# Kernel optimization log

Measured on AMD Instinct MI355X. Metric: run time of the kernel, lower is better.

## Reference

```python
import jax
import jax.numpy as jnp
import numpy as np
from jax import lax

B, NS, T, H, V = 4, 96, 8, 256, 32000
L = NS * T
N = NS + 1                    # num_nodes = num_statements + 1 (exit node)
NUM_LAYERS = NS // 16         # avg_statements_per_step = 16 -> 6 execution steps


def _lstm(c, h, x, Wx, Wh, b):
    """flax-style LSTM cell: gates in (i, f, g, o) order."""
    z = x @ Wx + h @ Wh + b
    gi, gf, gg, go = jnp.split(z, 4, axis=-1)
    c2 = jax.nn.sigmoid(gf) * c + jax.nn.sigmoid(gi) * jnp.tanh(gg)
    h2 = jax.nn.sigmoid(go) * jnp.tanh(c2)
    return c2, h2


def _forward(code_statements, code_length, embed, Wx_s, Wh_s, b_s, W_se, b_se,
             Wx_e, Wh_e, b_e, W_hk, b_hk, W_sd, b_sd, W_d1, b_d1, init_a, init_b):
    # ---- statement embedding: LSTM over the T tokens of each statement ----
    tok = embed[code_statements.astype(jnp.int32)]            # [B, L, H]
    tok = jnp.transpose(tok.reshape(B * NS, T, H), (1, 0, 2))  # [T, B*NS, H]
    c0 = jnp.zeros((B * NS, H), tok.dtype)

    def scan_fn(carry, x):
        c, hh = carry
        c, hh = _lstm(c, hh, x, Wx_s, Wh_s, b_s)
        return (c, hh), None

    (_, h_last), _ = lax.scan(scan_fn, (c0, c0), tok)
    stmt = h_last.reshape(B, NS, H)                           # [B, NS, H]

    # ---- skip encoder: pairwise segment-sum embedding for skipping i -> j ----
    node = jnp.concatenate([stmt, jnp.zeros((B, 1, H), stmt.dtype)], axis=1)  # [B,N,H]
    pref = jnp.concatenate(
        [jnp.zeros((B, 1, H), stmt.dtype), jnp.cumsum(node, axis=1)], axis=1)[:, :N]
    skip = (pref[:, None, :, :] - pref[:, :, None, :]) @ W_se + b_se  # [B,N,N,H]

    stmt_len = (code_length // T).astype(jnp.int32)           # exit node index per example

    # ---- execution loop with soft instruction pointer ----
    c = jnp.broadcast_to(init_a, (B, N, H))
    h = jnp.broadcast_to(init_b, (B, N, H))
    p = jnp.zeros((B, N)).at[:, 0].set(1.0)

    def step(c, h, p, skip_nnh, length, layer):
        # per-example: c,h [N,H]; p [N]; skip_nnh [N,N,H]; length scalar
        n = p.shape[0]
        ar = jnp.arange(n)
        if layer == 0:
            mask = jnp.zeros((n, n)).at[:, 1].set(1.0)
        elif layer == NUM_LAYERS - 1:
            mask = jnp.zeros((n, n)).at[:, length].set(1.0)   # force skip to exit
        else:
            mask = 1.0 - jnp.tri(n)                           # strictly forward skips
            mask = jnp.where(ar <= length, mask, 0.0)         # no skips past exit
            mask = mask.at[:, length].set(1.0)                # always allow exit

        # skip attention logits
        skip_keys = skip_nnh @ W_sd + b_sd                    # [N,N,H]
        h_key = h @ W_hk + b_hk                               # [N,H]
        act = jax.nn.relu(jnp.concatenate(
            [jnp.broadcast_to(h_key[:, None, :], (n, n, H)), skip_keys], axis=-1))
        skip_logits = jnp.squeeze(act @ W_d1, -1) + b_d1[0]   # [N,N]
        skip_logits = jnp.where(mask > 0, skip_logits, -jnp.inf)
        skip_p = jax.nn.softmax(skip_logits, axis=-1)

        # one LSTM skip-execution step for every (i, j) pair, vectorized
        z = skip_nnh @ Wx_e + (h @ Wh_e)[:, None, :] + b_e    # [N,N,4H]
        gi, gf, gg, go = jnp.split(z, 4, axis=-1)
        c_prop = jax.nn.sigmoid(gf) * c[:, None, :] + jax.nn.sigmoid(gi) * jnp.tanh(gg)
        h_prop = jax.nn.sigmoid(go) * jnp.tanh(c_prop)
        fwd_edge = (ar[None, :] > ar[:, None])[:, :, None]    # only j > i executes
        c_prop = jnp.where(fwd_edge, c_prop, c[:, None, :])
        h_prop = jnp.where(fwd_edge, h_prop, h[:, None, :])
        valid = (mask[:, :, None] > 0) & (p[:, None, None] > 0)
        c_prop = jnp.where(valid, c_prop, 0.0)
        h_prop = jnp.where(valid, h_prop, 0.0)

        # soft aggregation of proposals weighted by p(i) * skip_p(i -> j)
        w = skip_p * p[:, None]                               # [N,N]
        denom = (w.sum(axis=0) + 1e-7)[:, None]               # [N,1]
        c_new = jnp.einsum('ijh,ij->jh', c_prop, w) / denom
        h_new = jnp.einsum('ijh,ij->jh', h_prop, w) / denom
        p_new = p @ skip_p
        return c_new, h_new, p_new

    for layer in range(NUM_LAYERS):
        c, h, p = jax.vmap(step, in_axes=(0, 0, 0, 0, 0, None))(
            c, h, p, skip, stmt_len, layer)
    return h                                                  # [B, N, H]


def setup_inputs() -> dict:
    key = jax.random.key(0)
    ks = jax.random.split(key, 16)

    def dense(k, fi, fo):
        return jax.random.normal(k, (fi, fo)) * (1.0 / np.sqrt(fi))

    return {
        'code_statements': jax.random.randint(ks[0], (B, L), 0, V, dtype=jnp.int32),
        'code_length': jax.random.randint(ks[1], (B,), 64, L, dtype=jnp.int32),
        'embed': jax.random.normal(ks[2], (V, H)) * 0.02,
        'Wx_s': dense(ks[3], H, 4 * H), 'Wh_s': dense(ks[4], H, 4 * H),
        'b_s': jnp.zeros((4 * H,)),
        'W_se': dense(ks[5], H, H), 'b_se': jnp.zeros((H,)),
        'Wx_e': dense(ks[6], H, 4 * H), 'Wh_e': dense(ks[7], H, 4 * H),
        'b_e': jnp.zeros((4 * H,)),
        'W_hk': dense(ks[8], H, H), 'b_hk': jnp.zeros((H,)),
        'W_sd': dense(ks[9], H, H), 'b_sd': jnp.zeros((H,)),
        'W_d1': dense(ks[10], 2 * H, 1), 'b_d1': jnp.zeros((1,)),
        'init_a': jax.random.normal(ks[11], (H,)),
        'init_b': jax.random.normal(ks[12], (H,)),
    }


def reference(code_statements, code_length, embed, Wx_s, Wh_s, b_s, W_se, b_se,
              Wx_e, Wh_e, b_e, W_hk, b_hk, W_sd, b_sd, W_d1, b_d1, init_a, init_b):
    return _forward(code_statements, code_length, embed, Wx_s, Wh_s, b_s, W_se, b_se,
                    Wx_e, Wh_e, b_e, W_hk, b_hk, W_sd, b_sd, W_d1, b_d1, init_a, init_b)
```

## Files before the change

### kernel.cpp

```cpp
#include <hip/hip_runtime.h>
#include <cstddef>

#define B_   4
#define NS_  96
#define T_   8
#define H_   256
#define N_   97
#define NL_  6
#define R_   388

__device__ __forceinline__ float sigm(float x) {
    return __builtin_amdgcn_rcpf(1.0f + __builtin_amdgcn_exp2f(-1.44269504f * x));
}
__device__ __forceinline__ float tanh_f(float x) {
    return 1.0f - 2.0f * __builtin_amdgcn_rcpf(1.0f + __builtin_amdgcn_exp2f(2.88539008f * x));
}

__device__ __forceinline__ void fma16(float4 a, float4 w0, float4 w1, float4 w2,
                                      float4 w3, float* acc) {
    acc[0] = fmaf(a.x, w0.x, acc[0]); acc[1] = fmaf(a.x, w0.y, acc[1]);
    acc[2] = fmaf(a.x, w0.z, acc[2]); acc[3] = fmaf(a.x, w0.w, acc[3]);
    acc[0] = fmaf(a.y, w1.x, acc[0]); acc[1] = fmaf(a.y, w1.y, acc[1]);
    acc[2] = fmaf(a.y, w1.z, acc[2]); acc[3] = fmaf(a.y, w1.w, acc[3]);
    acc[0] = fmaf(a.z, w2.x, acc[0]); acc[1] = fmaf(a.z, w2.y, acc[1]);
    acc[2] = fmaf(a.z, w2.z, acc[2]); acc[3] = fmaf(a.z, w2.w, acc[3]);
    acc[0] = fmaf(a.w, w3.x, acc[0]); acc[1] = fmaf(a.w, w3.y, acc[1]);
    acc[2] = fmaf(a.w, w3.z, acc[2]); acc[3] = fmaf(a.w, w3.w, acc[3]);
}

__global__ __launch_bounds__(512, 4) void prologue(
        const int* __restrict__ ids, const float* __restrict__ embed,
        const float* __restrict__ Wx_s, const float* __restrict__ b_s,
        const float* __restrict__ b_se, const float* __restrict__ Wx_e,
        const float* __restrict__ b_e, const float* __restrict__ W_sd,
        const float* __restrict__ b_sd, const float* __restrict__ Wh_e,
        const float* __restrict__ init_a, const float* __restrict__ init_b,
        float* __restrict__ xz, float* __restrict__ cz, float* __restrict__ ck,
        float* __restrict__ hw, float* __restrict__ c0, float* __restrict__ h0,
        float* __restrict__ p0) {
    int bid = blockIdx.x, t = threadIdx.x;
    if (bid < 384) {
        __shared__ float As[64][260];
        __shared__ int ridx[64];
        int r0 = (bid >> 3) * 64, n0 = (bid & 7) * 128;
        if (t < 64) ridx[t] = ids[r0 + t];
        __syncthreads();
#pragma unroll
        for (int m = 0; m < 8; m++) {
            int L = m * 512 + t;
            int r = L >> 6, c4 = (L & 63) * 4;
            *(float4*)&As[r][c4] = *(const float4*)(embed + (size_t)ridx[r] * 256 + c4);
        }
        __syncthreads();
        int rg = t >> 5, cg = t & 31;
        float acc[4][4] = {};
        const float* wp = Wx_s + n0 + 4 * cg;
#pragma unroll 4
        for (int kb = 0; kb < 64; kb++) {
            float4 w0 = *(const float4*)(wp + (size_t)(4 * kb + 0) * 1024);
            float4 w1 = *(const float4*)(wp + (size_t)(4 * kb + 1) * 1024);
            float4 w2 = *(const float4*)(wp + (size_t)(4 * kb + 2) * 1024);
            float4 w3 = *(const float4*)(wp + (size_t)(4 * kb + 3) * 1024);
#pragma unroll
            for (int i = 0; i < 4; i++) {
                float4 a = *(const float4*)&As[rg * 4 + i][4 * kb];
                fma16(a, w0, w1, w2, w3, acc[i]);
            }
        }
        int col = n0 + 4 * cg;
        float4 bv = *(const float4*)&b_s[col];
#pragma unroll
        for (int i = 0; i < 4; i++) {
            int r = r0 + rg * 4 + i;
            float4 o = make_float4(acc[i][0] + bv.x, acc[i][1] + bv.y,
                                   acc[i][2] + bv.z, acc[i][3] + bv.w);
            *(float4*)&xz[(size_t)r * 1024 + col] = o;
        }
    } else if (bid < 386) {
        int n = (bid - 384) * 512 + t;
        float acc = b_e[n];
        for (int k = 0; k < 256; k++) acc = fmaf(b_se[k], Wx_e[(size_t)k * 1024 + n], acc);
        cz[n] = acc;
    } else if (bid < 388) {
        int n = (bid - 386) * 512 + t;
        float acc = b_e[n];
        for (int k = 0; k < 256; k++) {
            acc = fmaf(b_se[k], Wx_e[(size_t)k * 1024 + n], acc);
            acc = fmaf(init_b[k], Wh_e[(size_t)k * 1024 + n], acc);
        }
        hw[n] = acc;
    } else if (bid == 388) {
        if (t < 256) {
            float acc = b_sd[t];
            for (int k = 0; k < 256; k++) acc = fmaf(b_se[k], W_sd[(size_t)k * 256 + t], acc);
            ck[t] = acc;
        }
    } else {
        int r0 = (bid - 389) * 8 + (t >> 8) * 4;
        int col = t & 255;
        float ia = init_a[col], ib = init_b[col];
#pragma unroll
        for (int rr = 0; rr < 4; rr++) {
            int row = r0 + rr;
            if (row < R_) {
                c0[(size_t)row * 256 + col] = ia;
                h0[(size_t)row * 256 + col] = ib;
                if (col == 0) p0[row] = ((row % N_) == 0) ? 1.0f : 0.0f;
            }
        }
    }
}

__global__ __launch_bounds__(1024) void lstm_onepass(const float* __restrict__ xz,
        const float* __restrict__ Wh, float* __restrict__ hbuf) {
    __shared__ float zpart[4][2][1024];
    __shared__ float h_s[2][260];
    __shared__ float Wh_c[28][1024];
    int t = threadIdx.x;
    int s0 = blockIdx.x * 2;
    int kg = t >> 8, tg = t & 255;
    int sg = (t >> 8) & 1, cc = t & 255;
#pragma unroll
    for (int m = 0; m < 7; m++) {
        int L = m * 1024 + t;
        int r = L >> 8, c4 = (L & 255) * 4;
        *(float4*)&Wh_c[r][c4] = *(const float4*)(Wh + (size_t)r * 1024 + c4);
    }
    float creg = 0.0f, hreg = 0.0f;
    if (t < 512) {
        const float* z0 = xz + ((size_t)(s0 + sg) * T_) * 1024;
        float gi = z0[cc], gg = z0[512 + cc], go = z0[768 + cc];
        creg = sigm(gi) * tanh_f(gg);
        hreg = sigm(go) * tanh_f(creg);
        h_s[sg][cc] = hreg;
    }
    __syncthreads();
    for (int step = 1; step < T_; step++) {
        float x0 = 0.f, x1 = 0.f, x2 = 0.f, x3 = 0.f;
        if (t < 512) {
            const float* xzp = xz + ((size_t)(s0 + sg) * T_ + step) * 1024;
            x0 = xzp[cc]; x1 = xzp[256 + cc]; x2 = xzp[512 + cc]; x3 = xzp[768 + cc];
        }
        float4 z[2] = {};
        const float* wp = Wh + (size_t)(kg * 64) * 1024 + 4 * tg;
        int kbase = kg * 64;
        if (kg == 0) {
#pragma unroll
            for (int kb = 0; kb < 7; kb++) {
                float4 w0 = *(const float4*)&Wh_c[4 * kb + 0][4 * tg];
                float4 w1 = *(const float4*)&Wh_c[4 * kb + 1][4 * tg];
                float4 w2 = *(const float4*)&Wh_c[4 * kb + 2][4 * tg];
                float4 w3 = *(const float4*)&Wh_c[4 * kb + 3][4 * tg];
                int k = 4 * kb;
#pragma unroll
                for (int s = 0; s < 2; s++) {
                    float4 a = *(const float4*)&h_s[s][k];
                    fma16(a, w0, w1, w2, w3, (float*)&z[s]);
                }
            }
#pragma unroll 3
            for (int kb = 7; kb < 16; kb++) {
                float4 w0 = *(const float4*)(wp + (size_t)(4 * kb + 0) * 1024);
                float4 w1 = *(const float4*)(wp + (size_t)(4 * kb + 1) * 1024);
                float4 w2 = *(const float4*)(wp + (size_t)(4 * kb + 2) * 1024);
                float4 w3 = *(const float4*)(wp + (size_t)(4 * kb + 3) * 1024);
                int k = 4 * kb;
#pragma unroll
                for (int s = 0; s < 2; s++) {
                    float4 a = *(const float4*)&h_s[s][k];
                    fma16(a, w0, w1, w2, w3, (float*)&z[s]);
                }
            }
        } else {
#pragma unroll 4
            for (int kb = 0; kb < 16; kb++) {
                float4 w0 = *(const float4*)(wp + (size_t)(4 * kb + 0) * 1024);
                float4 w1 = *(const float4*)(wp + (size_t)(4 * kb + 1) * 1024);
                float4 w2 = *(const float4*)(wp + (size_t)(4 * kb + 2) * 1024);
                float4 w3 = *(const float4*)(wp + (size_t)(4 * kb + 3) * 1024);
                int k = kbase + 4 * kb;
#pragma unroll
                for (int s = 0; s < 2; s++) {
                    float4 a = *(const float4*)&h_s[s][k];
                    fma16(a, w0, w1, w2, w3, (float*)&z[s]);
                }
            }
        }
#pragma unroll
        for (int s = 0; s < 2; s++)
            *(float4*)&zpart[kg][s][4 * tg] = z[s];
        __syncthreads();
        if (t < 512) {
            float zv0 = x0 + zpart[0][sg][cc] + zpart[1][sg][cc]
                      + zpart[2][sg][cc] + zpart[3][sg][cc];
            float zv1 = x1 + zpart[0][sg][256 + cc] + zpart[1][sg][256 + cc]
                      + zpart[2][sg][256 + cc] + zpart[3][sg][256 + cc];
            float zv2 = x2 + zpart[0][sg][512 + cc] + zpart[1][sg][512 + cc]
                      + zpart[2][sg][512 + cc] + zpart[3][sg][512 + cc];
            float zv3 = x3 + zpart[0][sg][768 + cc] + zpart[1][sg][768 + cc]
                      + zpart[2][sg][768 + cc] + zpart[3][sg][768 + cc];
            creg = sigm(zv1) * creg + sigm(zv0) * tanh_f(zv2);
            hreg = sigm(zv3) * tanh_f(creg);
            h_s[sg][cc] = hreg;
        }
        __syncthreads();
    }
    if (t < 512) hbuf[(size_t)(s0 + sg) * H_ + cc] = hreg;
}

template<int MT>
__global__ __launch_bounds__(256) void gemm_t(const float* __restrict__ A,
        const float* __restrict__ W, const float* __restrict__ bias,
        const float* __restrict__ subQ, const float* __restrict__ pgate,
        float* __restrict__ C, int R, int NC) {
    __shared__ float As[MT][260];
    __shared__ int anyflag;
    int t = threadIdx.x;
    int n0 = blockIdx.x * 128;
    int r0 = blockIdx.y * MT;
    if (pgate) {
        if (t == 0) anyflag = 0;
        __syncthreads();
        if (t < MT && r0 + t < R && pgate[r0 + t] != 0.0f) anyflag = 1;
        __syncthreads();
        if (!anyflag) return;
    }
#pragma unroll
    for (int m = 0; m < MT / 4; m++) {
        int L = m * 256 + t;
        int r = L >> 6, c4 = (L & 63) * 4;
        int rr = r0 + r;
        float4 v = make_float4(0.f, 0.f, 0.f, 0.f);
        if (rr < R) v = *(const float4*)(A + (size_t)rr * 256 + c4);
        *(float4*)&As[r][c4] = v;
    }
    __syncthreads();
    constexpr int RT = MT / 8;
    int rg = t >> 5, cg = t & 31;
    float acc[RT][4] = {};
    const float* wp = W + n0 + 4 * cg;
#pragma unroll 2
    for (int kb = 0; kb < 64; kb++) {
        float4 w0 = *(const float4*)(wp + (size_t)(4 * kb + 0) * NC);
        float4 w1 = *(const float4*)(wp + (size_t)(4 * kb + 1) * NC);
        float4 w2 = *(const float4*)(wp + (size_t)(4 * kb + 2) * NC);
        float4 w3 = *(const float4*)(wp + (size_t)(4 * kb + 3) * NC);
#pragma unroll
        for (int i = 0; i < RT; i++) {
            float4 a = *(const float4*)&As[rg * RT + i][4 * kb];
            fma16(a, w0, w1, w2, w3, acc[i]);
        }
    }
    int col = n0 + 4 * cg;
    float4 bv = make_float4(0.f, 0.f, 0.f, 0.f);
    if (bias) bv = *(const float4*)&bias[col];
#pragma unroll
    for (int i = 0; i < RT; i++) {
        int r = r0 + rg * RT + i;
        if (r < R) {
            float4 o = make_float4(acc[i][0] + bv.x, acc[i][1] + bv.y,
                                   acc[i][2] + bv.z, acc[i][3] + bv.w);
            if (subQ) {
                float4 s4 = *(const float4*)(subQ + (size_t)r * NC + col);
                o.x -= s4.x; o.y -= s4.y; o.z -= s4.z; o.w -= s4.w;
            }
            *(float4*)&C[(size_t)r * NC + col] = o;
        }
    }
}

__global__ __launch_bounds__(256) void qr_kernel(const float* __restrict__ S,
        const float* __restrict__ Wx_e, const float* __restrict__ W_sd,
        const float* __restrict__ hw, float* __restrict__ q, float* __restrict__ ve0,
        float* __restrict__ r_, float* __restrict__ rT) {
    __shared__ float As[16][260];
    int t = threadIdx.x;
    int bx = blockIdx.x;
    int r0 = blockIdx.y * 16;
#pragma unroll
    for (int m = 0; m < 4; m++) {
        int L = m * 256 + t;
        int r = L >> 6, c4 = (L & 63) * 4;
        int rr = r0 + r;
        float4 v = make_float4(0.f, 0.f, 0.f, 0.f);
        if (rr < R_) v = *(const float4*)(S + (size_t)rr * 256 + c4);
        *(float4*)&As[r][c4] = v;
    }
    __syncthreads();
    bool isq = bx < 8;
    const float* W = isq ? Wx_e : W_sd;
    int NC = isq ? 1024 : 256;
    int n0 = (isq ? bx : bx - 8) * 128;
    int rg = t >> 5, cg = t & 31;
    float acc[2][4] = {};
    const float* wp = W + n0 + 4 * cg;
#pragma unroll 2
    for (int kb = 0; kb < 64; kb++) {
        float4 w0 = *(const float4*)(wp + (size_t)(4 * kb + 0) * NC);
        float4 w1 = *(const float4*)(wp + (size_t)(4 * kb + 1) * NC);
        float4 w2 = *(const float4*)(wp + (size_t)(4 * kb + 2) * NC);
        float4 w3 = *(const float4*)(wp + (size_t)(4 * kb + 3) * NC);
#pragma unroll
        for (int i = 0; i < 2; i++) {
            float4 a = *(const float4*)&As[rg * 2 + i][4 * kb];
            fma16(a, w0, w1, w2, w3, acc[i]);
        }
    }
    int col = n0 + 4 * cg;
#pragma unroll
    for (int i = 0; i < 2; i++) {
        int r = r0 + rg * 2 + i;
        if (r < R_) {
            float4 o = make_float4(acc[i][0], acc[i][1], acc[i][2], acc[i][3]);
            if (isq) {
                *(float4*)&q[(size_t)r * 1024 + col] = o;
                float4 hwv = *(const float4*)&hw[col];
                float4 v0 = make_float4(hwv.x - o.x, hwv.y - o.y, hwv.z - o.z, hwv.w - o.w);
                *(float4*)&ve0[(size_t)r * 1024 + col] = v0;
            } else {
                *(float4*)&r_[(size_t)r * 256 + col] = o;
                int b = r / N_, n = r - b * N_;
                rT[((size_t)b * 256 + col + 0) * 128 + n] = o.x;
                rT[((size_t)b * 256 + col + 1) * 128 + n] = o.y;
                rT[((size_t)b * 256 + col + 2) * 128 + n] = o.z;
                rT[((size_t)b * 256 + col + 3) * 128 + n] = o.w;
            }
        }
    }
}

__global__ __launch_bounds__(1024) void cumsum_k(const float* __restrict__ stmt,
                                                 float* __restrict__ pref) {
    __shared__ float buf[96][256];
    int b = blockIdx.x, t = threadIdx.x;
#pragma unroll
    for (int m = 0; m < 6; m++) {
        int L = m * 1024 + t;
        int r = L >> 6, c4 = (L & 63) * 4;
        *(float4*)&buf[r][c4] = *(const float4*)(stmt + ((size_t)b * NS_ + r) * 256 + c4);
    }
    __syncthreads();
    if (t < 256) {
        float run = 0.0f;
        pref[((size_t)b * N_) * H_ + t] = 0.0f;
        for (int n = 1; n < N_; n++) {
            run += buf[n - 1][t];
            pref[((size_t)b * N_ + n) * H_ + t] = run;
        }
    }
}

__global__ void softmax_once(const float* __restrict__ r, const float* __restrict__ rT,
                             const float* __restrict__ ck, const float* __restrict__ Wd1,
                             const int* __restrict__ code_length,
                             float* __restrict__ spT_mid, float* __restrict__ spT0,
                             float* __restrict__ spT5) {
    __shared__ float ri[H_], ckl[H_], wd[H_];
    __shared__ float part[8][128];
    __shared__ float red[4];
    int t = threadIdx.x;
    int j = t & 127, half = t >> 7;
    int bi = blockIdx.x;
    int b = bi / N_, i = bi % N_;
    if (t < H_) {
        ri[t] = r[(size_t)bi * H_ + t];
        ckl[t] = ck[t];
        wd[t] = Wd1[256 + t];
    }
    __syncthreads();
    int len = code_length[b] / T_;
    bool valid = (j < N_) && ((j > i && j <= len) || (j == len));
    float acc = 0.0f;
    if (valid) {
        const float* rTb = rT + (size_t)b * H_ * 128 + j;
        int h0 = half * 32;
#pragma unroll 4
        for (int hh = 0; hh < 32; hh++) {
            int h = h0 + hh;
            float v = rTb[(size_t)h * 128] - ri[h] + ckl[h];
            acc = fmaf(fmaxf(v, 0.0f), wd[h], acc);
        }
    }
    part[half][j] = acc;
    __syncthreads();
    float logit = -3.0e38f;
    if (t < 128) {
        if (valid)
            logit = part[0][j] + part[1][j] + part[2][j] + part[3][j]
                  + part[4][j] + part[5][j] + part[6][j] + part[7][j];
        float m = logit;
#pragma unroll
        for (int off = 32; off; off >>= 1) m = fmaxf(m, __shfl_xor(m, off));
        if ((t & 63) == 0) red[t >> 6] = m;
    }
    __syncthreads();
    float e = 0.0f;
    if (t < 128) {
        float m = fmaxf(red[0], red[1]);
        e = valid ? __builtin_amdgcn_exp2f(1.44269504f * (logit - m)) : 0.0f;
        float s = e;
#pragma unroll
        for (int off = 32; off; off >>= 1) s += __shfl_xor(s, off);
        if ((t & 63) == 0) red[2 + (t >> 6)] = s;
    }
    __syncthreads();
    if (t < 128 && j < N_) {
        float s = red[2] + red[3];
        size_t o = ((size_t)b * N_ + j) * 128 + i;
        spT_mid[o] = e / s;
        spT0[o] = (j == 1) ? 1.0f : 0.0f;
        spT5[o] = (j == len) ? 1.0f : 0.0f;
    }
}

__global__ __launch_bounds__(512) void aggregate(const float* __restrict__ q,
        const float* __restrict__ ve, const float* __restrict__ spT,
        const float* __restrict__ p, const float* __restrict__ cc,
        const float* __restrict__ hc, float* __restrict__ cn,
        float* __restrict__ hn, float* __restrict__ pn) {
    __shared__ float qj[1024];
    __shared__ float wcol[128];
    __shared__ int vlist[128];
    __shared__ int cnts[2];
    __shared__ float wsums[2];
    __shared__ float parts[2][2][H_];
    int t = threadIdx.x;
    int bj = blockIdx.x;
    int b = bj / N_, j = bj - b * N_;
    bool pred = false;
    int rank = 0;
    if (t < 128) {
        float wv = (t < N_) ? spT[(size_t)bj * 128 + t] * p[b * N_ + t] : 0.f;
        wcol[t] = wv;
        float s = wv;
#pragma unroll
        for (int off = 32; off; off >>= 1) s += __shfl_xor(s, off);
        pred = (wv != 0.0f);
        unsigned long long mask = __ballot(pred);
        int lane = t & 63;
        rank = __popcll(mask & ((1ull << lane) - 1ull));
        if (lane == 0) { cnts[t >> 6] = (int)__popcll(mask); wsums[t >> 6] = s; }
    }
    __syncthreads();
    float wsum = wsums[0] + wsums[1];
    int nv = cnts[0] + cnts[1];
    if (t < 128 && pred) vlist[(t >= 64 ? cnts[0] : 0) + rank] = t;
    if (wsum == 0.0f) {
        if (t < 256) {
            cn[(size_t)bj * H_ + t] = 0.0f;
            hn[(size_t)bj * H_ + t] = 0.0f;
            if (t == 0) pn[bj] = 0.0f;
        }
        return;
    }
    qj[t] = q[(size_t)bj * 1024 + t];
    qj[512 + t] = q[(size_t)bj * 1024 + 512 + t];
    __syncthreads();
    int hh = t & 255, vs = t >> 8;
    float ac = 0.f, ah = 0.f;
    for (int v = vs; v < nv; v += 2) {
        int i = vlist[v];
        float wv = wcol[i];
        size_t rowi = (size_t)b * N_ + i;
        if (j > i) {
            const float* vei = ve + rowi * 1024;
            float gi = qj[hh] + vei[hh];
            float gf = qj[256 + hh] + vei[256 + hh];
            float gg = qj[512 + hh] + vei[512 + hh];
            float go = qj[768 + hh] + vei[768 + hh];
            float c2 = cc[rowi * H_ + hh];
            float cp = sigm(gf) * c2 + sigm(gi) * tanh_f(gg);
            float hp = sigm(go) * tanh_f(cp);
            ac = fmaf(wv, cp, ac);
            ah = fmaf(wv, hp, ah);
        } else {
            ac = fmaf(wv, cc[rowi * H_ + hh], ac);
            ah = fmaf(wv, hc[rowi * H_ + hh], ah);
        }
    }
    parts[vs][0][hh] = ac;
    parts[vs][1][hh] = ah;
    __syncthreads();
    if (t < 256) {
        float inv = __builtin_amdgcn_rcpf(wsum + 1e-7f);
        cn[(size_t)bj * H_ + t] = (parts[0][0][t] + parts[1][0][t]) * inv;
        hn[(size_t)bj * H_ + t] = (parts[0][1][t] + parts[1][1][t]) * inv;
        if (t == 0) pn[bj] = wsum;
    }
}


extern "C" void kernel_launch(void* const* d_in, const int* in_sizes, int n_in,
                              void* d_out, int out_size, void* d_ws, size_t ws_size,
                              hipStream_t stream) {
    const int*   code_statements = (const int*)d_in[0];
    const int*   code_length = (const int*)d_in[1];
    const float* embed = (const float*)d_in[2];
    const float* Wx_s = (const float*)d_in[3];
    const float* Wh_s = (const float*)d_in[4];
    const float* b_s  = (const float*)d_in[5];
    const float* W_se = (const float*)d_in[6];
    const float* b_se = (const float*)d_in[7];
    const float* Wx_e = (const float*)d_in[8];
    const float* Wh_e = (const float*)d_in[9];
    const float* b_e  = (const float*)d_in[10];
    const float* W_sd = (const float*)d_in[13];
    const float* b_sd = (const float*)d_in[14];
    const float* W_d1 = (const float*)d_in[15];
    const float* init_a = (const float*)d_in[17];
    const float* init_b = (const float*)d_in[18];
    float* out = (float*)d_out;

    float* wsf = (float*)d_ws;
    size_t off = 0;
    auto alloc = [&](size_t n) { float* p = wsf + off; off += n; return p; };
    float* cz = alloc(1024);
    float* ck = alloc(256);
    float* hw = alloc(1024);
    float* xz = alloc((size_t)3072 * 1024);
    float* stmt = alloc(384 * 256);
    float* pref = alloc(R_ * 256);
    float* s_   = alloc(R_ * 256);
    float* q  = alloc(R_ * 1024);
    float* r_ = alloc(R_ * 256);
    float* rT = alloc(4 * 256 * 128);
    float* ve = alloc(R_ * 1024);
    float* spT_mid = alloc(R_ * 128);
    float* spT0    = alloc(R_ * 128);
    float* spT5    = alloc(R_ * 128);
    float* p0 = alloc(R_);
    float* p1 = alloc(R_);
    float* c0 = alloc(R_ * 256);
    float* c1 = alloc(R_ * 256);
    float* h0 = alloc(R_ * 256);
    float* h1 = alloc(R_ * 256);

    prologue<<<dim3(438), 512, 0, stream>>>(code_statements, embed, Wx_s, b_s,
                                            b_se, Wx_e, b_e, W_sd, b_sd, Wh_e,
                                            init_a, init_b, xz, cz, ck, hw, c0, h0, p0);
    lstm_onepass<<<dim3(192), 1024, 0, stream>>>(xz, Wh_s, stmt);
    cumsum_k<<<dim3(4), 1024, 0, stream>>>(stmt, pref);
    gemm_t<16><<<dim3(2, 25), 256, 0, stream>>>(pref, W_se, nullptr, nullptr, nullptr,
                                                s_, R_, 256);
    qr_kernel<<<dim3(10, 25), 256, 0, stream>>>(s_, Wx_e, W_sd, hw, q, ve, r_, rT);
    softmax_once<<<dim3(R_), 1024, 0, stream>>>(r_, rT, ck, W_d1, code_length,
                                                spT_mid, spT0, spT5);

    for (int layer = 0; layer < NL_; layer++) {
        bool odd = (layer & 1);
        float* pc = odd ? p1 : p0;
        float* pn = odd ? p0 : p1;
        float* cc = odd ? c1 : c0;
        float* cn = odd ? c0 : c1;
        float* hc = odd ? h1 : h0;
        float* hn = odd ? h0 : h1;
        if (layer == NL_ - 1) hn = out;
        const float* spT = (layer == 0) ? spT0 : (layer == NL_ - 1) ? spT5 : spT_mid;
        aggregate<<<dim3(R_), 512, 0, stream>>>(q, ve, spT, pc, cc, hc, cn, hn, pn);
        if (layer < NL_ - 1)
            gemm_t<16><<<dim3(8, 25), 256, 0, stream>>>(hn, Wh_e, cz, q, pn,
                                                        ve, R_, 1024);
    }
}
```

Before: 372.5 us.

## Reassociate skip projection through prefix sums and specialize layer zero analytically

New measurement: 348.6 us. 6.4% less time.

```diff
diff --git a/kernel.cpp b/kernel.cpp
--- a/kernel.cpp
+++ b/kernel.cpp
@@ -34,10 +34,9 @@
         const float* __restrict__ b_se, const float* __restrict__ Wx_e,
         const float* __restrict__ b_e, const float* __restrict__ W_sd,
         const float* __restrict__ b_sd, const float* __restrict__ Wh_e,
-        const float* __restrict__ init_a, const float* __restrict__ init_b,
+        const float* __restrict__ W_se, const float* __restrict__ init_b,
         float* __restrict__ xz, float* __restrict__ cz, float* __restrict__ ck,
-        float* __restrict__ hw, float* __restrict__ c0, float* __restrict__ h0,
-        float* __restrict__ p0) {
+        float* __restrict__ hw, float* __restrict__ Mbuf) {
     int bid = blockIdx.x, t = threadIdx.x;
     if (bid < 384) {
         __shared__ float As[64][260];
@@ -76,37 +75,62 @@
                                    acc[i][2] + bv.z, acc[i][3] + bv.w);
             *(float4*)&xz[(size_t)r * 1024 + col] = o;
         }
-    } else if (bid < 386) {
-        int n = (bid - 384) * 512 + t;
+    } else if (bid < 424) {
+        __shared__ float As[64][260];
+        bool isM1 = bid < 416;
+        int mb = isM1 ? bid - 384 : bid - 416;
+        int r0m = isM1 ? (mb >> 3) * 64 : (mb >> 1) * 64;
+        int n0 = isM1 ? (mb & 7) * 128 : (mb & 1) * 128;
+        const float* W = isM1 ? Wx_e : W_sd;
+        int NC = isM1 ? 1024 : 256;
+        int cbase = isM1 ? 0 : 1024;
+#pragma unroll
+        for (int m = 0; m < 8; m++) {
+            int L = m * 512 + t;
+            int r = L >> 6, c4 = (L & 63) * 4;
+            *(float4*)&As[r][c4] = *(const float4*)(W_se + (size_t)(r0m + r) * 256 + c4);
+        }
+        __syncthreads();
+        int rg = t >> 5, cg = t & 31;
+        float acc[4][4] = {};
+        const float* wp = W + n0 + 4 * cg;
+#pragma unroll 4
+        for (int kb = 0; kb < 64; kb++) {
+            float4 w0 = *(const float4*)(wp + (size_t)(4 * kb + 0) * NC);
+            float4 w1 = *(const float4*)(wp + (size_t)(4 * kb + 1) * NC);
+            float4 w2 = *(const float4*)(wp + (size_t)(4 * kb + 2) * NC);
+            float4 w3 = *(const float4*)(wp + (size_t)(4 * kb + 3) * NC);
+#pragma unroll
+            for (int i = 0; i < 4; i++) {
+                float4 a = *(const float4*)&As[rg * 4 + i][4 * kb];
+                fma16(a, w0, w1, w2, w3, acc[i]);
+            }
+        }
+        int col = cbase + n0 + 4 * cg;
+#pragma unroll
+        for (int i = 0; i < 4; i++) {
+            int r = r0m + rg * 4 + i;
+            *(float4*)&Mbuf[(size_t)r * 1280 + col] =
+                make_float4(acc[i][0], acc[i][1], acc[i][2], acc[i][3]);
+        }
+    } else if (bid < 426) {
+        int n = (bid - 424) * 512 + t;
         float acc = b_e[n];
         for (int k = 0; k < 256; k++) acc = fmaf(b_se[k], Wx_e[(size_t)k * 1024 + n], acc);
         cz[n] = acc;
-    } else if (bid < 388) {
-        int n = (bid - 386) * 512 + t;
+    } else if (bid < 428) {
+        int n = (bid - 426) * 512 + t;
         float acc = b_e[n];
         for (int k = 0; k < 256; k++) {
             acc = fmaf(b_se[k], Wx_e[(size_t)k * 1024 + n], acc);
             acc = fmaf(init_b[k], Wh_e[(size_t)k * 1024 + n], acc);
         }
         hw[n] = acc;
-    } else if (bid == 388) {
+    } else {
         if (t < 256) {
             float acc = b_sd[t];
             for (int k = 0; k < 256; k++) acc = fmaf(b_se[k], W_sd[(size_t)k * 256 + t], acc);
             ck[t] = acc;
-        }
-    } else {
-        int r0 = (bid - 389) * 8 + (t >> 8) * 4;
-        int col = t & 255;
-        float ia = init_a[col], ib = init_b[col];
-#pragma unroll
-        for (int rr = 0; rr < 4; rr++) {
-            int row = r0 + rr;
-            if (row < R_) {
-                c0[(size_t)row * 256 + col] = ia;
-                h0[(size_t)row * 256 + col] = ib;
-                if (col == 0) p0[row] = ((row % N_) == 0) ? 1.0f : 0.0f;
-            }
         }
     }
 }
@@ -269,83 +293,34 @@
     }
 }
 
-__global__ __launch_bounds__(256) void qr_kernel(const float* __restrict__ S,
-        const float* __restrict__ Wx_e, const float* __restrict__ W_sd,
+__global__ __launch_bounds__(256) void scan_wide(const float* __restrict__ y2,
         const float* __restrict__ hw, float* __restrict__ q, float* __restrict__ ve0,
         float* __restrict__ r_, float* __restrict__ rT) {
-    __shared__ float As[16][260];
-    int t = threadIdx.x;
-    int bx = blockIdx.x;
-    int r0 = blockIdx.y * 16;
-#pragma unroll
-    for (int m = 0; m < 4; m++) {
-        int L = m * 256 + t;
-        int r = L >> 6, c4 = (L & 63) * 4;
-        int rr = r0 + r;
-        float4 v = make_float4(0.f, 0.f, 0.f, 0.f);
-        if (rr < R_) v = *(const float4*)(S + (size_t)rr * 256 + c4);
-        *(float4*)&As[r][c4] = v;
-    }
-    __syncthreads();
-    bool isq = bx < 8;
-    const float* W = isq ? Wx_e : W_sd;
-    int NC = isq ? 1024 : 256;
-    int n0 = (isq ? bx : bx - 8) * 128;
-    int rg = t >> 5, cg = t & 31;
-    float acc[2][4] = {};
-    const float* wp = W + n0 + 4 * cg;
-#pragma unroll 2
-    for (int kb = 0; kb < 64; kb++) {
-        float4 w0 = *(const float4*)(wp + (size_t)(4 * kb + 0) * NC);
-        float4 w1 = *(const float4*)(wp + (size_t)(4 * kb + 1) * NC);
-        float4 w2 = *(const float4*)(wp + (size_t)(4 * kb + 2) * NC);
-        float4 w3 = *(const float4*)(wp + (size_t)(4 * kb + 3) * NC);
-#pragma unroll
-        for (int i = 0; i < 2; i++) {
-            float4 a = *(const float4*)&As[rg * 2 + i][4 * kb];
-            fma16(a, w0, w1, w2, w3, acc[i]);
-        }
-    }
-    int col = n0 + 4 * cg;
-#pragma unroll
-    for (int i = 0; i < 2; i++) {
-        int r = r0 + rg * 2 + i;
-        if (r < R_) {
-            float4 o = make_float4(acc[i][0], acc[i][1], acc[i][2], acc[i][3]);
-            if (isq) {
-                *(float4*)&q[(size_t)r * 1024 + col] = o;
-                float4 hwv = *(const float4*)&hw[col];
-                float4 v0 = make_float4(hwv.x - o.x, hwv.y - o.y, hwv.z - o.z, hwv.w - o.w);
-                *(float4*)&ve0[(size_t)r * 1024 + col] = v0;
-            } else {
-                *(float4*)&r_[(size_t)r * 256 + col] = o;
-                int b = r / N_, n = r - b * N_;
-                rT[((size_t)b * 256 + col + 0) * 128 + n] = o.x;
-                rT[((size_t)b * 256 + col + 1) * 128 + n] = o.y;
-                rT[((size_t)b * 256 + col + 2) * 128 + n] = o.z;
-                rT[((size_t)b * 256 + col + 3) * 128 + n] = o.w;
-            }
-        }
-    }
-}
-
-__global__ __launch_bounds__(1024) void cumsum_k(const float* __restrict__ stmt,
-                                                 float* __restrict__ pref) {
-    __shared__ float buf[96][256];
-    int b = blockIdx.x, t = threadIdx.x;
-#pragma unroll
-    for (int m = 0; m < 6; m++) {
-        int L = m * 1024 + t;
-        int r = L >> 6, c4 = (L & 63) * 4;
-        *(float4*)&buf[r][c4] = *(const float4*)(stmt + ((size_t)b * NS_ + r) * 256 + c4);
-    }
-    __syncthreads();
-    if (t < 256) {
+    int bid = blockIdx.x, t = threadIdx.x;
+    int b = bid / 5, ch = bid - b * 5;
+    int ccol = ch * 256 + t;
+    const float* yp = y2 + (size_t)b * 96 * 1280 + ccol;
+    if (ccol < 1024) {
+        float hwv = hw[ccol];
+        float* qp = q + (size_t)b * N_ * 1024 + ccol;
+        float* vp = ve0 + (size_t)b * N_ * 1024 + ccol;
+        qp[0] = 0.0f; vp[0] = hwv;
         float run = 0.0f;
-        pref[((size_t)b * N_) * H_ + t] = 0.0f;
         for (int n = 1; n < N_; n++) {
-            run += buf[n - 1][t];
-            pref[((size_t)b * N_ + n) * H_ + t] = run;
+            run += yp[(size_t)(n - 1) * 1280];
+            qp[(size_t)n * 1024] = run;
+            vp[(size_t)n * 1024] = hwv - run;
+        }
+    } else {
+        int rc = ccol - 1024;
+        float* rp = r_ + (size_t)b * N_ * 256 + rc;
+        float* rtp = rT + ((size_t)b * 256 + rc) * 128;
+        rp[0] = 0.0f; rtp[0] = 0.0f;
+        float run = 0.0f;
+        for (int n = 1; n < N_; n++) {
+            run += yp[(size_t)(n - 1) * 1280];
+            rp[(size_t)n * 256] = run;
+            rtp[n] = run;
         }
     }
 }
@@ -353,14 +328,42 @@
 __global__ void softmax_once(const float* __restrict__ r, const float* __restrict__ rT,
                              const float* __restrict__ ck, const float* __restrict__ Wd1,
                              const int* __restrict__ code_length,
-                             float* __restrict__ spT_mid, float* __restrict__ spT0,
-                             float* __restrict__ spT5) {
+                             float* __restrict__ spT_mid, float* __restrict__ spT5,
+                             const float* __restrict__ hw, const float* __restrict__ cz,
+                             const float* __restrict__ init_a,
+                             const float* __restrict__ Wh_e, const float* __restrict__ q,
+                             float* __restrict__ ve, float* __restrict__ c1,
+                             float* __restrict__ h1, float* __restrict__ p1) {
     __shared__ float ri[H_], ckl[H_], wd[H_];
     __shared__ float part[8][128];
     __shared__ float red[4];
     int t = threadIdx.x;
+    int bi = blockIdx.x;
+    if (bi >= R_) {
+        int b = bi - R_;
+        const float* q1 = q + (size_t)(b * N_ + 1) * 1024;
+        if (t < 256) {
+            float gi = q1[t] + hw[t];
+            float gf = q1[256 + t] + hw[256 + t];
+            float gg = q1[512 + t] + hw[512 + t];
+            float go = q1[768 + t] + hw[768 + t];
+            float cpr = sigm(gf) * init_a[t] + sigm(gi) * tanh_f(gg);
+            float hpr = sigm(go) * tanh_f(cpr);
+            float sc = __builtin_amdgcn_rcpf(1.0f + 1e-7f);
+            float hpv = hpr * sc;
+            c1[(size_t)(b * N_ + 1) * 256 + t] = cpr * sc;
+            h1[(size_t)(b * N_ + 1) * 256 + t] = hpv;
+            ri[t] = hpv;
+            if (t < N_) p1[b * N_ + t] = (t == 1) ? 1.0f : 0.0f;
+        }
+        __syncthreads();
+        float acc = cz[t] - q1[t];
+        for (int k = 0; k < 256; k++)
+            acc = fmaf(ri[k], Wh_e[(size_t)k * 1024 + t], acc);
+        ve[(size_t)(b * N_ + 1) * 1024 + t] = acc;
+        return;
+    }
     int j = t & 127, half = t >> 7;
-    int bi = blockIdx.x;
     int b = bi / N_, i = bi % N_;
     if (t < H_) {
         ri[t] = r[(size_t)bi * H_ + t];
@@ -408,7 +411,6 @@
         float s = red[2] + red[3];
         size_t o = ((size_t)b * N_ + j) * 128 + i;
         spT_mid[o] = e / s;
-        spT0[o] = (j == 1) ? 1.0f : 0.0f;
         spT5[o] = (j == len) ? 1.0f : 0.0f;
     }
 }
@@ -519,14 +521,13 @@
     float* hw = alloc(1024);
     float* xz = alloc((size_t)3072 * 1024);
     float* stmt = alloc(384 * 256);
-    float* pref = alloc(R_ * 256);
-    float* s_   = alloc(R_ * 256);
+    float* Mbuf = alloc(256 * 1280);
+    float* y2   = alloc((size_t)384 * 1280);
     float* q  = alloc(R_ * 1024);
     float* r_ = alloc(R_ * 256);
     float* rT = alloc(4 * 256 * 128);
     float* ve = alloc(R_ * 1024);
     float* spT_mid = alloc(R_ * 128);
-    float* spT0    = alloc(R_ * 128);
     float* spT5    = alloc(R_ * 128);
     float* p0 = alloc(R_);
     float* p1 = alloc(R_);
@@ -535,18 +536,18 @@
     float* h0 = alloc(R_ * 256);
     float* h1 = alloc(R_ * 256);
 
-    prologue<<<dim3(438), 512, 0, stream>>>(code_statements, embed, Wx_s, b_s,
+    prologue<<<dim3(429), 512, 0, stream>>>(code_statements, embed, Wx_s, b_s,
                                             b_se, Wx_e, b_e, W_sd, b_sd, Wh_e,
-                                            init_a, init_b, xz, cz, ck, hw, c0, h0, p0);
+                                            W_se, init_b, xz, cz, ck, hw, Mbuf);
     lstm_onepass<<<dim3(192), 1024, 0, stream>>>(xz, Wh_s, stmt);
-    cumsum_k<<<dim3(4), 1024, 0, stream>>>(stmt, pref);
-    gemm_t<16><<<dim3(2, 25), 256, 0, stream>>>(pref, W_se, nullptr, nullptr, nullptr,
-                                                s_, R_, 256);
-    qr_kernel<<<dim3(10, 25), 256, 0, stream>>>(s_, Wx_e, W_sd, hw, q, ve, r_, rT);
-    softmax_once<<<dim3(R_), 1024, 0, stream>>>(r_, rT, ck, W_d1, code_length,
-                                                spT_mid, spT0, spT5);
-
-    for (int layer = 0; layer < NL_; layer++) {
+    gemm_t<16><<<dim3(10, 24), 256, 0, stream>>>(stmt, Mbuf, nullptr, nullptr, nullptr,
+                                                 y2, 384, 1280);
+    scan_wide<<<dim3(20), 256, 0, stream>>>(y2, hw, q, ve, r_, rT);
+    softmax_once<<<dim3(R_ + B_), 1024, 0, stream>>>(r_, rT, ck, W_d1, code_length,
+                                                     spT_mid, spT5, hw, cz, init_a,
+                                                     Wh_e, q, ve, c1, h1, p1);
+
+    for (int layer = 1; layer < NL_; layer++) {
         bool odd = (layer & 1);
         float* pc = odd ? p1 : p0;
         float* pn = odd ? p0 : p1;
@@ -555,7 +556,7 @@
         float* hc = odd ? h1 : h0;
         float* hn = odd ? h0 : h1;
         if (layer == NL_ - 1) hn = out;
-        const float* spT = (layer == 0) ? spT0 : (layer == NL_ - 1) ? spT5 : spT_mid;
+        const float* spT = (layer == NL_ - 1) ? spT5 : spT_mid;
         aggregate<<<dim3(R_), 512, 0, stream>>>(q, ve, spT, pc, cc, hc, cn, hn, pn);
         if (layer < NL_ - 1)
             gemm_t<16><<<dim3(8, 25), 256, 0, stream>>>(hn, Wh_e, cz, q, pn,
```
